# Kernel optimization log

Measured on AMD Instinct MI355X. Metric: run time of the kernel, lower is better.

## Reference

```python
import jax, jax.numpy as jnp
from jax import lax
import numpy as np

LAM = 0.2
MAX_ITER = 10
EPS = 1e-07
WIN_SIZE = 2
COS_EPS = 1e-5
L, B, D = 1024, 32, 256


def setup_inputs() -> dict:
    key = jax.random.key(0)
    k1, k2, k3 = jax.random.split(key, 3)
    m1 = jax.random.normal(k1, (L, B, D), dtype=jnp.float32)
    m2 = jax.random.normal(k2, (L, B, D), dtype=jnp.float32)
    lengths = jax.random.randint(k3, (B,), L // 2, L + 1, dtype=jnp.int32)
    return {"m1": m1, "m2": m2, "lengths": lengths}


def _sinkhorn_item(x, y, l):
    # x, y: (L, D) padded; l: scalar valid length
    Lm = x.shape[0]
    idx = jnp.arange(Lm)
    mask = idx < l                              # (L,) valid rows/cols
    mm = mask[:, None] & mask[None, :]          # (L, L) valid block

    # cosine distance: 1 - cos_sim with eps clamp (matches nn.CosineSimilarity)
    xn = x / jnp.maximum(jnp.linalg.norm(x, axis=-1, keepdims=True), COS_EPS)
    yn = y / jnp.maximum(jnp.linalg.norm(y, axis=-1, keepdims=True), COS_EPS)
    M = 1.0 - xn @ yn.T                          # (L, L)
    # band penalty: +100 outside |i-j| <= win_size
    band = jnp.abs(idx[:, None] - idx[None, :]) > WIN_SIZE
    M = M + 100.0 * band

    lf = l.astype(M.dtype)
    r = jnp.where(mask, 1.0 / lf, 0.0)           # row marginals 1/n on valid prefix
    c = r                                        # col marginals (n == m == l)

    P = jnp.exp(-LAM * M) * mm
    P = P / jnp.sum(P)
    u0 = jnp.zeros(Lm, dtype=M.dtype)

    def step(carry, _):
        P, u, active = carry
        usum = jnp.sum(P, axis=1)
        cond = active & (jnp.max(jnp.abs(u - usum)) > EPS)
        u_new = usum
        scale_r = jnp.where(mask, r / jnp.where(mask, u_new, 1.0), 0.0)
        P1 = P * scale_r[:, None]
        s = jnp.sum(P1, axis=0)
        # NOTE: original torch code reshapes (c / P.sum(0)) to (-1, 1), i.e.
        # applies the column-sum correction along ROWS (works since n == m).
        # We reproduce that exactly for faithfulness.
        scale_c = jnp.where(mask, c / jnp.where(mask, s, 1.0), 0.0)
        P2 = P1 * scale_c[:, None]
        P_out = jnp.where(cond, P2, P)
        u_out = jnp.where(cond, u_new, u)
        return (P_out, u_out, cond), None

    (P, _, _), _ = lax.scan(step, (P, u0, jnp.array(True)), None, length=MAX_ITER)

    # final: P / P.sum(-1)  -- torch broadcasting divides column j by rowsum[j]
    rowsum = jnp.sum(P, axis=-1)
    rs = jnp.where(mask, rowsum, 1.0)
    P_norm = jnp.where(mm, P / rs[None, :], 0.0)
    cost = jnp.sum(P * M)
    return P_norm, cost


def _forward(m1, m2, lengths):
    # m1, m2: (L, B, D) -> vmap over batch axis 1
    f = jax.vmap(_sinkhorn_item, in_axes=(1, 1, 0))
    P, cost = f(m1, m2, lengths)                 # (B, L, L), (B,)
    return P, cost


def reference(m1, m2, lengths):
    return _forward(m1, m2, lengths)
```

## Files before the change

kernel.cpp:

```cpp
#include <hip/hip_runtime.h>
#include <math.h>

#define L 1024
#define NB 32
#define DD 256
#define LAM_F 0.2f
#define EPS_F 1e-7f

#define NDBLK (NB * (L / 16))
#define FILLBLK (NB * L * L / 4 / 1024)

__device__ __forceinline__ float wave_sum(float v) {
#pragma unroll
    for (int m = 1; m < 64; m <<= 1) v += __shfl_xor(v, m, 64);
    return v;
}
__device__ __forceinline__ float wave_max(float v) {
#pragma unroll
    for (int m = 1; m < 64; m <<= 1) v = fmaxf(v, __shfl_xor(v, m, 64));
    return v;
}
__device__ __forceinline__ float dot4(float4 a, float4 b) {
    return a.x * b.x + a.y * b.y + a.z * b.z + a.w * b.w;
}

__global__ void __launch_bounds__(1024) prep_kernel(
        const float* __restrict__ m1, const float* __restrict__ m2,
        float* __restrict__ dots, float* __restrict__ xn2o, float* __restrict__ yn2o,
        float* __restrict__ out) {
    if (blockIdx.x >= NDBLK) {
        size_t t = (size_t)(blockIdx.x - NDBLK) * 1024 + threadIdx.x;
        ((float4*)out)[t] = make_float4(0.f, 0.f, 0.f, 0.f);
        return;
    }
    __shared__ float ysh[20 * DD];
    const int b = blockIdx.x >> 6;
    const int i0 = (blockIdx.x & 63) << 4;
    for (int f = threadIdx.x; f < 20 * (DD / 4); f += 1024) {
        int srow = f >> 6, l4 = f & 63;
        int j = i0 - 2 + srow;
        if (j >= 0 && j < L)
            ((float4*)ysh)[f] = ((const float4*)(m2 + (size_t)(j * NB + b) * DD))[l4];
    }
    __syncthreads();
    const int w = threadIdx.x >> 6, lane = threadIdx.x & 63;
    const int i = i0 + w;
    const float4 xv = ((const float4*)(m1 + (size_t)(i * NB + b) * DD))[lane];
    float xn2 = dot4(xv, xv);
    const float4 yself = ((const float4*)(ysh + (w + 2) * DD))[lane];
    float yn2 = dot4(yself, yself);
    float dt[5];
#pragma unroll
    for (int o = 0; o < 5; ++o) {
        int j = i + o - 2;
        float d = 0.f;
        if (j >= 0 && j < L) {
            const float4 y2 = ((const float4*)(ysh + (w + o) * DD))[lane];
            d = dot4(xv, y2);
        }
        dt[o] = d;
    }
    xn2 = wave_sum(xn2);
    yn2 = wave_sum(yn2);
#pragma unroll
    for (int o = 0; o < 5; ++o) dt[o] = wave_sum(dt[o]);
    if (lane == 0) {
        const int r = b * L + i;
        xn2o[r] = xn2;
        yn2o[r] = yn2;
#pragma unroll
        for (int o = 0; o < 5; ++o) dots[r * 5 + o] = dt[o];
    }
}

__global__ void __launch_bounds__(64) sinkhorn_kernel(
        const float* __restrict__ dots, const float* __restrict__ xn2,
        const float* __restrict__ yn2, const int* __restrict__ lengths,
        float* __restrict__ out) {
    const int b = blockIdx.x;
    const int lane = threadIdx.x;
    const int l = lengths[b];
    const float rmarg = 1.0f / (float)l;
    const int r0 = lane << 4;

    float inv_nx[16], inv_ny[16];
#pragma unroll
    for (int k = 0; k < 16; ++k) {
        const int base = b * L + r0 + k;
        inv_nx[k] = 1.0f / fmaxf(sqrtf(xn2[base]), 1e-5f);
        inv_ny[k] = 1.0f / fmaxf(sqrtf(yn2[base]), 1e-5f);
    }
    float nyext[20];
    nyext[0] = __shfl_up(inv_ny[14], 1, 64);
    nyext[1] = __shfl_up(inv_ny[15], 1, 64);
#pragma unroll
    for (int k = 0; k < 16; ++k) nyext[k + 2] = inv_ny[k];
    nyext[18] = __shfl_down(inv_ny[0], 1, 64);
    nyext[19] = __shfl_down(inv_ny[1], 1, 64);

    float P0[16][5], p0sum[16], pm0[16];
#pragma unroll
    for (int k = 0; k < 16; ++k) {
        const int i = r0 + k;
        const int base = b * L + i;
        p0sum[k] = 0.f;
        pm0[k] = 0.f;
#pragma unroll
        for (int o = 0; o < 5; ++o) {
            const int j = i + o - 2;
            const float dv = dots[base * 5 + o];
            const float M = 1.0f - dv * inv_nx[k] * nyext[k + o];
            const bool valid = (j >= 0) && (j < L) && (i < l) && (j < l);
            const float P = valid ? expf(-LAM_F * M) : 0.0f;
            P0[k][o] = P;
            p0sum[k] += P;
            pm0[k] += P * M;
        }
    }
    float tot = 0.f;
#pragma unroll
    for (int k = 0; k < 16; ++k) tot += p0sum[k];
    tot = wave_sum(tot);
    const float inv_total = 1.0f / tot;
    float sacc[16], u[16];
#pragma unroll
    for (int k = 0; k < 16; ++k) { sacc[k] = inv_total; u[k] = 0.f; }

    const float pA = __shfl_up(P0[14][4], 1, 64);
    const float pB = __shfl_up(P0[15][3], 1, 64);
    const float pC = __shfl_up(P0[15][4], 1, 64);
    const float pE = __shfl_down(P0[0][0], 1, 64);
    const float pD = __shfl_down(P0[0][1], 1, 64);
    const float pF = __shfl_down(P0[1][0], 1, 64);

    for (int it = 0; it < 10; ++it) {
        float us[16], diff = 0.f;
#pragma unroll
        for (int k = 0; k < 16; ++k) {
            us[k] = p0sum[k] * sacc[k];
            diff = fmaxf(diff, fabsf(u[k] - us[k]));
        }
        diff = wave_max(diff);
        if (diff <= EPS_F) break;

        float s1[16];
#pragma unroll
        for (int k = 0; k < 16; ++k) {
            u[k] = us[k];
            const float sr = (r0 + k < l) ? rmarg / us[k] : 0.0f;
            s1[k] = sacc[k] * sr;
        }
        float s1ext[20];
        {
            float a = __shfl_up(s1[14], 1, 64), c = __shfl_up(s1[15], 1, 64);
            float d = __shfl_down(s1[0], 1, 64), e = __shfl_down(s1[1], 1, 64);
            s1ext[0] = (lane == 0) ? 0.f : a;
            s1ext[1] = (lane == 0) ? 0.f : c;
            s1ext[18] = (lane == 63) ? 0.f : d;
            s1ext[19] = (lane == 63) ? 0.f : e;
        }
#pragma unroll
        for (int k = 0; k < 16; ++k) s1ext[k + 2] = s1[k];

        float s[16];
#pragma unroll
        for (int k = 0; k < 16; ++k) {
            float acc = P0[k][2] * s1ext[k + 2];
            acc += ((k >= 2) ? P0[k - 2][4] : ((k == 0) ? pA : pC)) * s1ext[k];
            acc += ((k >= 1) ? P0[k - 1][3] : pB) * s1ext[k + 1];
            acc += ((k <= 14) ? P0[k + 1][1] : pD) * s1ext[k + 3];
            acc += ((k <= 13) ? P0[k + 2][0] : ((k == 14) ? pE : pF)) * s1ext[k + 4];
            s[k] = acc;
        }
#pragma unroll
        for (int k = 0; k < 16; ++k) {
            const float sc = (r0 + k < l) ? rmarg / s[k] : 0.0f;
            sacc[k] = s1[k] * sc;
        }
    }

    float rs[16];
#pragma unroll
    for (int k = 0; k < 16; ++k) rs[k] = (r0 + k < l) ? p0sum[k] * sacc[k] : 1.0f;
    float rsext[20];
    rsext[0] = __shfl_up(rs[14], 1, 64);
    rsext[1] = __shfl_up(rs[15], 1, 64);
#pragma unroll
    for (int k = 0; k < 16; ++k) rsext[k + 2] = rs[k];
    rsext[18] = __shfl_down(rs[0], 1, 64);
    rsext[19] = __shfl_down(rs[1], 1, 64);

    float cpart = 0.f;
#pragma unroll
    for (int k = 0; k < 16; ++k) cpart += pm0[k] * sacc[k];
    cpart = wave_sum(cpart);
    if (lane == 0) out[(size_t)NB * L * L + b] = cpart;

#pragma unroll
    for (int k = 0; k < 16; ++k) {
        const int i = r0 + k;
        const float pv0 = P0[k][0] * sacc[k] / rsext[k + 0];
        const float pv1 = P0[k][1] * sacc[k] / rsext[k + 1];
        const float pv2 = P0[k][2] * sacc[k] / rsext[k + 2];
        const float pv3 = P0[k][3] * sacc[k] / rsext[k + 3];
        const float pv4 = P0[k][4] * sacc[k] / rsext[k + 4];
        const int c0 = (i - 2 > 0 ? i - 2 : 0) >> 2;
        const int c1 = (i + 2 < L - 1 ? i + 2 : L - 1) >> 2;
        float4* orow = (float4*)(out + ((size_t)b * L + i) * L);
        for (int c = c0; c <= c1; ++c) {
            float e[4];
#pragma unroll
            for (int t = 0; t < 4; ++t) {
                const int o = 4 * c + t - i + 2;
                e[t] = (o == 0) ? pv0 : (o == 1) ? pv1 : (o == 2) ? pv2
                       : (o == 3) ? pv3 : (o == 4) ? pv4 : 0.0f;
            }
            orow[c] = make_float4(e[0], e[1], e[2], e[3]);
        }
    }
}

extern "C" void kernel_launch(void* const* d_in, const int* in_sizes, int n_in,
                              void* d_out, int out_size, void* d_ws, size_t ws_size,
                              hipStream_t stream) {
    const float* m1 = (const float*)d_in[0];
    const float* m2 = (const float*)d_in[1];
    const int* lengths = (const int*)d_in[2];
    float* out = (float*)d_out;
    float* ws = (float*)d_ws;

    float* dots = ws;
    float* xn2 = dots + NB * L * 5;
    float* yn2 = xn2 + NB * L;

    prep_kernel<<<NDBLK + FILLBLK, 1024, 0, stream>>>(m1, m2, dots, xn2, yn2, out);
    sinkhorn_kernel<<<NB, 64, 0, stream>>>(dots, xn2, yn2, lengths, out);
}
```

Measured before the change: 200.2 us.

## Overlap zero-fill of output with Sinkhorn solve in one launch

Moves the output zero-fill out of the dot-product kernel and into the solve kernel as extra blocks, each writing only the float4s outside the band. The 32 latency-bound solver blocks now run concurrently with the bandwidth-bound fill instead of after it. The band region is no longer written twice. The risk is that fill blocks compete with the solver blocks for scheduling.

```diff
diff --git a/kernel.cpp b/kernel.cpp
--- a/kernel.cpp
+++ b/kernel.cpp
@@ -8,7 +8,8 @@
 #define EPS_F 1e-7f
 
 #define NDBLK (NB * (L / 16))
-#define FILLBLK (NB * L * L / 4 / 1024)
+#define NSINK NB
+#define NFILL 8192
 
 __device__ __forceinline__ float wave_sum(float v) {
 #pragma unroll
@@ -24,15 +25,9 @@
     return a.x * b.x + a.y * b.y + a.z * b.z + a.w * b.w;
 }
 
-__global__ void __launch_bounds__(1024) prep_kernel(
+__global__ void __launch_bounds__(1024) dots_kernel(
         const float* __restrict__ m1, const float* __restrict__ m2,
-        float* __restrict__ dots, float* __restrict__ xn2o, float* __restrict__ yn2o,
-        float* __restrict__ out) {
-    if (blockIdx.x >= NDBLK) {
-        size_t t = (size_t)(blockIdx.x - NDBLK) * 1024 + threadIdx.x;
-        ((float4*)out)[t] = make_float4(0.f, 0.f, 0.f, 0.f);
-        return;
-    }
+        float* __restrict__ dots, float* __restrict__ xn2o, float* __restrict__ yn2o) {
     __shared__ float ysh[20 * DD];
     const int b = blockIdx.x >> 6;
     const int i0 = (blockIdx.x & 63) << 4;
@@ -73,12 +68,29 @@
     }
 }
 
-__global__ void __launch_bounds__(64) sinkhorn_kernel(
+__global__ void __launch_bounds__(64) solve_fill_kernel(
         const float* __restrict__ dots, const float* __restrict__ xn2,
         const float* __restrict__ yn2, const int* __restrict__ lengths,
         float* __restrict__ out) {
+    const int lane = threadIdx.x;
+
+    if (blockIdx.x >= NSINK) {
+        const int t0 = (blockIdx.x - NSINK) << 10;
+#pragma unroll
+        for (int k = 0; k < 16; ++k) {
+            const int t = t0 + (k << 6) + lane;
+            const int rem = t & 262143;
+            const int i = rem >> 8;
+            const int c = rem & 255;
+            const int c0 = ((i - 2 > 0) ? i - 2 : 0) >> 2;
+            const int c1 = ((i + 2 < L - 1) ? i + 2 : L - 1) >> 2;
+            if (c < c0 || c > c1)
+                ((float4*)out)[t] = make_float4(0.f, 0.f, 0.f, 0.f);
+        }
+        return;
+    }
+
     const int b = blockIdx.x;
-    const int lane = threadIdx.x;
     const int l = lengths[b];
     const float rmarg = 1.0f / (float)l;
     const int r0 = lane << 4;
@@ -204,8 +216,8 @@
         const float pv2 = P0[k][2] * sacc[k] / rsext[k + 2];
         const float pv3 = P0[k][3] * sacc[k] / rsext[k + 3];
         const float pv4 = P0[k][4] * sacc[k] / rsext[k + 4];
-        const int c0 = (i - 2 > 0 ? i - 2 : 0) >> 2;
-        const int c1 = (i + 2 < L - 1 ? i + 2 : L - 1) >> 2;
+        const int c0 = ((i - 2 > 0) ? i - 2 : 0) >> 2;
+        const int c1 = ((i + 2 < L - 1) ? i + 2 : L - 1) >> 2;
         float4* orow = (float4*)(out + ((size_t)b * L + i) * L);
         for (int c = c0; c <= c1; ++c) {
             float e[4];
@@ -233,6 +245,6 @@
     float* xn2 = dots + NB * L * 5;
     float* yn2 = xn2 + NB * L;
 
-    prep_kernel<<<NDBLK + FILLBLK, 1024, 0, stream>>>(m1, m2, dots, xn2, yn2, out);
-    sinkhorn_kernel<<<NB, 64, 0, stream>>>(dots, xn2, yn2, lengths, out);
-}
+    dots_kernel<<<NDBLK, 1024, 0, stream>>>(m1, m2, dots, xn2, yn2);
+    solve_fill_kernel<<<NSINK + NFILL, 64, 0, stream>>>(dots, xn2, yn2, lengths, out);
+}
```

New measurement: 197.5 us. About the same (-1.3%).
